# Kernel optimization log

Hardware: AMD Instinct MI355X
Metric: run time of the kernel (lower is better)

## Reference

```python
import jax, jax.numpy as jnp
import numpy as np

B, N, M, DIM, H, DH = 2, 2048, 2048, 512, 8, 64
INNER = H * DH  # 512


def setup_inputs() -> dict:
    key = jax.random.key(0)
    ks = jax.random.split(key, 9)
    s = 0.02
    return {
        "x": jax.random.normal(ks[0], (B, N, DIM), jnp.float32),
        "x1": jax.random.normal(ks[1], (B, M, DIM), jnp.float32),
        "attn_mat": jax.random.normal(ks[2], (B, H, N, M), jnp.float32),
        "dots_para": jax.random.uniform(ks[3], (1,), jnp.float32),
        "mat_para": jax.random.uniform(ks[4], (1,), jnp.float32),
        "W_qv": jax.random.normal(ks[5], (DIM, 2 * INNER), jnp.float32) * s,
        "W_k": jax.random.normal(ks[6], (DIM, INNER), jnp.float32) * s,
        "W_out": jax.random.normal(ks[7], (INNER, DIM), jnp.float32) * s,
        "b_out": jax.random.normal(ks[8], (DIM,), jnp.float32) * s,
    }


def _split_heads(t):
    # [b, n, h*d] -> [b, h, n, d]
    b, n, _ = t.shape
    return t.reshape(b, n, H, DH).transpose(0, 2, 1, 3)


def reference(x, x1, attn_mat, dots_para, mat_para, W_qv, W_k, W_out, b_out):
    scale = DH ** -0.5
    qv = x @ W_qv                      # [b, n, 2*inner]
    q, v = jnp.split(qv, 2, axis=-1)
    q = _split_heads(q)                # [b, h, n, d]
    v = _split_heads(v)                # [b, h, n, d]
    k = _split_heads(x1 @ W_k)         # [b, h, m, d]
    dots = jnp.einsum("bhnd,bhmd->bhnm", q, k) * scale
    dots = dots * dots_para + attn_mat * mat_para
    attn = jax.nn.softmax(dots, axis=-1)
    out = jnp.einsum("bhnm,bhmd->bhnd", attn, v)
    out = out.transpose(0, 2, 1, 3).reshape(x.shape[0], x.shape[1], INNER)
    return out @ W_out + b_out
```

## Files before the change

### kernel.cpp

```cpp
#include <hip/hip_runtime.h>

#define NB 2048
#define MB 2048
#define SPLITS 4
#define MSP (MB / SPLITS)

typedef __attribute__((ext_vector_type(8))) short short8;
typedef __attribute__((ext_vector_type(4))) float floatx4;

__device__ __forceinline__ unsigned short f2bf(float f) {
    union { float f; unsigned int u; } v; v.f = f;
    unsigned int r = (v.u + 0x7FFFu + ((v.u >> 16) & 1u)) >> 16;
    return (unsigned short)r;
}

__device__ __forceinline__ int swz(int row, int k) {
    return (row << 6) + ((((k >> 3) ^ (row & 7))) << 3) + (k & 7);
}
__device__ __forceinline__ int vswz(int row, int k) {
    return (row << 6) + ((((k >> 3) ^ (row & 7) ^ ((row >> 3) & 7))) << 3) + (k & 7);
}

__device__ __forceinline__ void gload16(const unsigned short* g, short* l) {
    __builtin_amdgcn_global_load_lds(
        (const __attribute__((address_space(1))) void*)g,
        (__attribute__((address_space(3))) void*)l, 16, 0, 0);
}

__launch_bounds__(256)
__global__ void prep(const float* __restrict__ x, const float* __restrict__ x1,
                     const float* __restrict__ Wqv, const float* __restrict__ Wk,
                     const float* __restrict__ Wout,
                     unsigned short* __restrict__ xb, unsigned short* __restrict__ x1b,
                     unsigned short* __restrict__ Wqvt, unsigned short* __restrict__ Wkt,
                     unsigned short* __restrict__ Woutt) {
    __shared__ float t[64][65];
    const int bid = blockIdx.x, tid = threadIdx.x;
    if (bid < 2048) {
        const float* in = bid < 1024 ? x : x1;
        unsigned short* out = bid < 1024 ? xb : x1b;
        size_t off = ((size_t)(bid & 1023) * 256 + tid) * 8;
        float4 d0 = *(const float4*)(in + off);
        float4 d1 = *(const float4*)(in + off + 4);
        uint4 o;
        o.x = (unsigned int)f2bf(d0.x) | ((unsigned int)f2bf(d0.y) << 16);
        o.y = (unsigned int)f2bf(d0.z) | ((unsigned int)f2bf(d0.w) << 16);
        o.z = (unsigned int)f2bf(d1.x) | ((unsigned int)f2bf(d1.y) << 16);
        o.w = (unsigned int)f2bf(d1.z) | ((unsigned int)f2bf(d1.w) << 16);
        *(uint4*)(out + off) = o;
        return;
    }
    int tb = bid - 2048;
    const float* W; unsigned short* Wt; int N;
    if (tb < 128)      { W = Wqv;  Wt = Wqvt;  N = 1024; }
    else if (tb < 192) { tb -= 128; W = Wk;   Wt = Wkt;   N = 512; }
    else               { tb -= 192; W = Wout; Wt = Woutt; N = 512; }
    const int k0 = (tb & 7) * 64, n0 = (tb >> 3) * 64;
#pragma unroll
    for (int p = 0; p < 4; p++) {
        int idx = p * 256 + tid;
        int kr = idx >> 4, c4 = (idx & 15) << 2;
        float4 d = *(const float4*)(W + (size_t)(k0 + kr) * N + n0 + c4);
        t[kr][c4 + 0] = d.x; t[kr][c4 + 1] = d.y; t[kr][c4 + 2] = d.z; t[kr][c4 + 3] = d.w;
    }
    __syncthreads();
#pragma unroll
    for (int p = 0; p < 4; p++) {
        int idx = p * 256 + tid;
        int nr = idx >> 4, k4 = (idx & 15) << 2;
        uint2 o;
        o.x = (unsigned int)f2bf(t[k4 + 0][nr]) | ((unsigned int)f2bf(t[k4 + 1][nr]) << 16);
        o.y = (unsigned int)f2bf(t[k4 + 2][nr]) | ((unsigned int)f2bf(t[k4 + 3][nr]) << 16);
        *(uint2*)(Wt + (size_t)(n0 + nr) * 512 + k0 + k4) = o;
    }
}

template <int OUT_BF16>
__device__ __forceinline__ void gemm128_body(const unsigned short* __restrict__ A,
                                             const unsigned short* __restrict__ Bt,
                                             const float* __restrict__ bias,
                                             void* __restrict__ Cp, int Nc, int m0, int n0,
                                             short* Al, short* Bl) {
    const int tid = threadIdx.x;
    const int w = tid >> 6, lane = tid & 63;
    const int quad = lane >> 4, c16 = lane & 15;
    const int wr = (w >> 1) * 64, wc = (w & 1) * 64;

    floatx4 acc[4][4];
#pragma unroll
    for (int i = 0; i < 4; i++)
#pragma unroll
        for (int j = 0; j < 4; j++) acc[i][j] = floatx4{0.f, 0.f, 0.f, 0.f};

    const unsigned short* Ap = A + (size_t)m0 * 512;
    const unsigned short* Bp = Bt + (size_t)n0 * 512;

    for (int kk = 0; kk < 512; kk += 64) {
#pragma unroll
        for (int p = 0; p < 4; p++) {
            int idx = p * 256 + tid;
            int row = idx >> 3, c8 = (idx & 7) << 3;
            gload16(Ap + (size_t)row * 512 + kk + c8, Al + idx * 8);
            gload16(Bp + (size_t)row * 512 + kk + c8, Bl + idx * 8);
        }
        __syncthreads();
#pragma unroll
        for (int kc = 0; kc < 2; kc++) {
            short8 af[4], bf[4];
#pragma unroll
            for (int mt = 0; mt < 4; mt++)
                af[mt] = *(const short8*)&Al[(wr + mt * 16 + c16) * 64 + kc * 32 + quad * 8];
#pragma unroll
            for (int nt = 0; nt < 4; nt++)
                bf[nt] = *(const short8*)&Bl[(wc + nt * 16 + c16) * 64 + kc * 32 + quad * 8];
#pragma unroll
            for (int mt = 0; mt < 4; mt++)
#pragma unroll
                for (int nt = 0; nt < 4; nt++)
                    acc[mt][nt] = __builtin_amdgcn_mfma_f32_16x16x32_bf16(af[mt], bf[nt], acc[mt][nt], 0, 0, 0);
        }
        __syncthreads();
    }
#pragma unroll
    for (int mt = 0; mt < 4; mt++)
#pragma unroll
        for (int nt = 0; nt < 4; nt++)
#pragma unroll
            for (int r = 0; r < 4; r++) {
                int row = m0 + wr + mt * 16 + quad * 4 + r;
                int col = n0 + wc + nt * 16 + c16;
                float v = acc[mt][nt][r];
                if (OUT_BF16) {
                    ((unsigned short*)Cp)[(size_t)row * Nc + col] = f2bf(v);
                } else {
                    ((float*)Cp)[(size_t)row * Nc + col] = v + bias[col];
                }
            }
}

__launch_bounds__(256)
__global__ void gemm_qvk(const unsigned short* __restrict__ xb, const unsigned short* __restrict__ x1b,
                         const unsigned short* __restrict__ Wqvt, const unsigned short* __restrict__ Wkt,
                         unsigned short* __restrict__ qvbf, unsigned short* __restrict__ kbf) {
    __shared__ short Al[128 * 64];
    __shared__ short Bl[128 * 64];
    int bid = blockIdx.x;
    if (bid < 256) {
        gemm128_body<1>(xb, Wqvt, nullptr, qvbf, 1024, (bid & 31) * 128, (bid >> 5) * 128, Al, Bl);
    } else {
        bid -= 256;
        gemm128_body<1>(x1b, Wkt, nullptr, kbf, 512, (bid & 31) * 128, (bid >> 5) * 128, Al, Bl);
    }
}

__launch_bounds__(256)
__global__ void gemm_out(const unsigned short* __restrict__ A, const unsigned short* __restrict__ Bt,
                         const float* __restrict__ bias, float* __restrict__ C) {
    __shared__ short Al[128 * 64];
    __shared__ short Bl[128 * 64];
    gemm128_body<0>(A, Bt, bias, C, 512, blockIdx.x * 128, blockIdx.y * 128, Al, Bl);
}

__launch_bounds__(256)
__global__ void flash_attn(const unsigned short* __restrict__ qv,
                           const unsigned short* __restrict__ kb,
                           const float* __restrict__ attn_mat,
                           const float* __restrict__ dots_para,
                           const float* __restrict__ mat_para,
                           float* __restrict__ Opart,
                           float* __restrict__ lpart) {
    __shared__ short QP[4][32 * 64];
    __shared__ short Ks[2][64 * 64];
    __shared__ short Vs[2][64 * 64];

    const int tid = threadIdx.x, w = tid >> 6, lane = tid & 63;
    const int quad = lane >> 4, c16 = lane & 15;
    const int q0 = blockIdx.x * 128;
    const int bh = blockIdx.y;
    const int sp = blockIdx.z;
    const int b = bh >> 3, h = bh & 7;
    const int ms = sp * MSP;

    const float log2e = 1.4426950408889634f;
    const float mp = mat_para[0] * log2e;
    const float sdp = dots_para[0] * 0.125f * log2e;

    short* QPf = (short*)QP;
#pragma unroll
    for (int p = 0; p < 4; p++) {
        int id = p * 256 + tid;
        int r = id >> 3, c = id & 7;
        *(uint4*)&QPf[swz(r, c * 8)] =
            *(const uint4*)(qv + (size_t)(b * NB + q0 + r) * 1024 + h * 64 + c * 8);
    }
    __syncthreads();
    short8 qf[2][2];
#pragma unroll
    for (int at = 0; at < 2; at++)
#pragma unroll
        for (int kc = 0; kc < 2; kc++)
            qf[at][kc] = *(const short8*)&QPf[swz(w * 32 + at * 16 + c16, kc * 32 + quad * 8)];
    short* Pw = &QPf[w * 2048];

    const int sr = tid >> 3, sc = tid & 7;
    uint4 kreg[2], vreg[2];
    auto loadKV = [&](int m) {
#pragma unroll
        for (int p = 0; p < 2; p++) {
            int r = p * 32 + sr;
            kreg[p] = *(const uint4*)(kb + (size_t)(b * MB + m + r) * 512 + h * 64 + sc * 8);
            vreg[p] = *(const uint4*)(qv + (size_t)(b * NB + m + r) * 1024 + 512 + h * 64 + sc * 8);
        }
    };
    auto storeKV = [&](int bufi) {
#pragma unroll
        for (int p = 0; p < 2; p++) {
            int r = p * 32 + sr;
            *(uint4*)&Ks[bufi][swz(r, sc * 8)] = kreg[p];
            uint4 d = vreg[p];
            Vs[bufi][vswz(sc * 8 + 0, r)] = (short)(d.x & 0xffff);
            Vs[bufi][vswz(sc * 8 + 1, r)] = (short)(d.x >> 16);
            Vs[bufi][vswz(sc * 8 + 2, r)] = (short)(d.y & 0xffff);
            Vs[bufi][vswz(sc * 8 + 3, r)] = (short)(d.y >> 16);
            Vs[bufi][vswz(sc * 8 + 4, r)] = (short)(d.z & 0xffff);
            Vs[bufi][vswz(sc * 8 + 5, r)] = (short)(d.z >> 16);
            Vs[bufi][vswz(sc * 8 + 6, r)] = (short)(d.w & 0xffff);
            Vs[bufi][vswz(sc * 8 + 7, r)] = (short)(d.w >> 16);
        }
    };
    const float* amp = attn_mat + ((size_t)bh * NB + q0 + w * 32 + quad * 4) * MB + c16;
    float amr[2][4][4];
    auto loadAM = [&](int m0_) {
#pragma unroll
        for (int at = 0; at < 2; at++)
#pragma unroll
            for (int r = 0; r < 4; r++)
#pragma unroll
                for (int t = 0; t < 4; t++)
                    amr[at][t][r] = amp[(size_t)(at * 16 + r) * MB + m0_ + t * 16];
    };

    loadKV(ms);
    storeKV(0);
    loadKV(ms + 64 < ms + MSP ? ms + 64 : ms);
    loadAM(ms);

    floatx4 O[2][4];
    float l[2][4];
#pragma unroll
    for (int at = 0; at < 2; at++)
#pragma unroll
        for (int i = 0; i < 4; i++) { O[at][i] = floatx4{0.f, 0.f, 0.f, 0.f}; l[at][i] = 0.f; }

    for (int it = 0; it < MSP / 64; it++) {
        const int m0 = ms + it * 64;
        const int buf = it & 1, nbuf = buf ^ 1;
        __syncthreads();
        storeKV(nbuf);
        int mnn = m0 + 128; if (mnn >= ms + MSP) mnn = ms;
        loadKV(mnn);

        floatx4 S[2][4];
        __builtin_amdgcn_s_setprio(1);
#pragma unroll
        for (int t = 0; t < 4; t++) {
            short8 kf0 = *(const short8*)&Ks[buf][swz(t * 16 + c16, quad * 8)];
            short8 kf1 = *(const short8*)&Ks[buf][swz(t * 16 + c16, 32 + quad * 8)];
#pragma unroll
            for (int at = 0; at < 2; at++) {
                floatx4 s = floatx4{0.f, 0.f, 0.f, 0.f};
                s = __builtin_amdgcn_mfma_f32_16x16x32_bf16(qf[at][0], kf0, s, 0, 0, 0);
                s = __builtin_amdgcn_mfma_f32_16x16x32_bf16(qf[at][1], kf1, s, 0, 0, 0);
                S[at][t] = s;
            }
        }
        __builtin_amdgcn_s_setprio(0);

#pragma unroll
        for (int at = 0; at < 2; at++)
#pragma unroll
            for (int t = 0; t < 4; t++) {
                float p0 = exp2f(fmaf(S[at][t][0], sdp, amr[at][t][0] * mp));
                float p1 = exp2f(fmaf(S[at][t][1], sdp, amr[at][t][1] * mp));
                float p2 = exp2f(fmaf(S[at][t][2], sdp, amr[at][t][2] * mp));
                float p3 = exp2f(fmaf(S[at][t][3], sdp, amr[at][t][3] * mp));
                l[at][0] += p0; l[at][1] += p1; l[at][2] += p2; l[at][3] += p3;
                unsigned int w01, w23;
                asm("v_cvt_pk_bf16_f32 %0, %1, %2" : "=v"(w01) : "v"(p0), "v"(p1));
                asm("v_cvt_pk_bf16_f32 %0, %1, %2" : "=v"(w23) : "v"(p2), "v"(p3));
                int br = at * 16 + quad * 4;
                Pw[swz(br + 0, t * 16 + c16)] = (short)(w01 & 0xffff);
                Pw[swz(br + 1, t * 16 + c16)] = (short)(w01 >> 16);
                Pw[swz(br + 2, t * 16 + c16)] = (short)(w23 & 0xffff);
                Pw[swz(br + 3, t * 16 + c16)] = (short)(w23 >> 16);
            }
        int mnx = m0 + 64; if (mnx >= ms + MSP) mnx = ms;
        loadAM(mnx);
        __threadfence_block();

        short8 pf[2][2];
#pragma unroll
        for (int at = 0; at < 2; at++)
#pragma unroll
            for (int kc = 0; kc < 2; kc++)
                pf[at][kc] = *(const short8*)&Pw[swz(at * 16 + c16, kc * 32 + quad * 8)];
        __builtin_amdgcn_s_setprio(1);
#pragma unroll
        for (int dt = 0; dt < 4; dt++) {
            short8 vf0 = *(const short8*)&Vs[buf][vswz(dt * 16 + c16, quad * 8)];
            short8 vf1 = *(const short8*)&Vs[buf][vswz(dt * 16 + c16, 32 + quad * 8)];
#pragma unroll
            for (int at = 0; at < 2; at++) {
                O[at][dt] = __builtin_amdgcn_mfma_f32_16x16x32_bf16(pf[at][0], vf0, O[at][dt], 0, 0, 0);
                O[at][dt] = __builtin_amdgcn_mfma_f32_16x16x32_bf16(pf[at][1], vf1, O[at][dt], 0, 0, 0);
            }
        }
        __builtin_amdgcn_s_setprio(0);
    }

#pragma unroll
    for (int at = 0; at < 2; at++) {
#pragma unroll
        for (int r = 0; r < 4; r++) {
            float s = l[at][r];
            s += __shfl_xor(s, 1);
            s += __shfl_xor(s, 2);
            s += __shfl_xor(s, 4);
            s += __shfl_xor(s, 8);
            l[at][r] = s;
        }
        if (c16 == 0) {
#pragma unroll
            for (int r = 0; r < 4; r++)
                lpart[(size_t)(sp * 16 + bh) * NB + q0 + w * 32 + at * 16 + quad * 4 + r] = l[at][r];
        }
#pragma unroll
        for (int dt = 0; dt < 4; dt++)
#pragma unroll
            for (int r = 0; r < 4; r++) {
                size_t row = (size_t)sp * 4096 + b * NB + q0 + w * 32 + at * 16 + quad * 4 + r;
                Opart[row * 512 + h * 64 + dt * 16 + c16] = O[at][dt][r];
            }
    }
}

__launch_bounds__(256)
__global__ void combine_splits(const float* __restrict__ Opart, const float* __restrict__ lpart,
                               unsigned short* __restrict__ ao) {
    int idx = blockIdx.x * 256 + threadIdx.x;
    int row = idx >> 7;
    int col = (idx & 127) << 2;
    int b = row >> 11, n = row & 2047, h = col >> 6;
    float ls = 0.f;
    float4 o = {0.f, 0.f, 0.f, 0.f};
#pragma unroll
    for (int sp = 0; sp < SPLITS; sp++) {
        ls += lpart[(size_t)(sp * 16 + b * 8 + h) * NB + n];
        float4 os = *(const float4*)(Opart + ((size_t)sp * 4096 + row) * 512 + col);
        o.x += os.x; o.y += os.y; o.z += os.z; o.w += os.w;
    }
    float rinv = 1.0f / ls;
    uint2 pk;
    pk.x = (unsigned int)f2bf(o.x * rinv) | ((unsigned int)f2bf(o.y * rinv) << 16);
    pk.y = (unsigned int)f2bf(o.z * rinv) | ((unsigned int)f2bf(o.w * rinv) << 16);
    *(uint2*)(ao + (size_t)row * 512 + col) = pk;
}

extern "C" void kernel_launch(void* const* d_in, const int* in_sizes, int n_in,
                              void* d_out, int out_size, void* d_ws, size_t ws_size,
                              hipStream_t stream) {
    const float* x         = (const float*)d_in[0];
    const float* x1        = (const float*)d_in[1];
    const float* attn_mat  = (const float*)d_in[2];
    const float* dots_para = (const float*)d_in[3];
    const float* mat_para  = (const float*)d_in[4];
    const float* W_qv      = (const float*)d_in[5];
    const float* W_k       = (const float*)d_in[6];
    const float* W_out     = (const float*)d_in[7];
    const float* b_out     = (const float*)d_in[8];
    float* out = (float*)d_out;

    unsigned short* xb    = (unsigned short*)d_ws;
    unsigned short* x1b   = xb    + (size_t)4096 * 512;
    unsigned short* qvbf  = x1b   + (size_t)4096 * 512;
    unsigned short* kbf   = qvbf  + (size_t)4096 * 1024;
    unsigned short* aobf  = kbf   + (size_t)4096 * 512;
    unsigned short* Wqvt  = aobf  + (size_t)4096 * 512;
    unsigned short* Wkt   = Wqvt  + (size_t)1024 * 512;
    unsigned short* Woutt = Wkt   + (size_t)512 * 512;
    float*          Opart = (float*)(Woutt + (size_t)512 * 512);
    float*          lpart = Opart + (size_t)SPLITS * 4096 * 512;

    dim3 blk(256);
    prep<<<2304, blk, 0, stream>>>(x, x1, W_qv, W_k, W_out, xb, x1b, Wqvt, Wkt, Woutt);
    gemm_qvk<<<384, blk, 0, stream>>>(xb, x1b, Wqvt, Wkt, qvbf, kbf);
    flash_attn<<<dim3(16, 16, SPLITS), blk, 0, stream>>>(qvbf, kbf, attn_mat, dots_para, mat_para, Opart, lpart);
    combine_splits<<<2048, blk, 0, stream>>>(Opart, lpart, aobf);
    gemm_out<<<dim3(32, 4), blk, 0, stream>>>(aobf, Woutt, b_out, out);
}
```

Baseline: 439.3 us.

## Double-buffer GEMMs with swizzled async LDS loads and halve N tile

The GEMM body now double-buffers A/B tiles in LDS using direct global-to-LDS loads with an XOR-swizzled layout, which removes one barrier per k-step and avoids bank conflicts. The N tile shrinks from 128 to 64 so twice as many blocks launch for the QVK and output GEMMs. In flash attention, Q and K tiles also use direct swizzled global-to-LDS loads instead of going through registers, while V still goes through registers for its transpose. The changes trade more LDS per block and smaller per-wave tiles for better latency hiding and more parallelism.

```diff
diff --git a/kernel.cpp b/kernel.cpp
--- a/kernel.cpp
+++ b/kernel.cpp
@@ -76,59 +76,73 @@
 }
 
 template <int OUT_BF16>
-__device__ __forceinline__ void gemm128_body(const unsigned short* __restrict__ A,
-                                             const unsigned short* __restrict__ Bt,
-                                             const float* __restrict__ bias,
-                                             void* __restrict__ Cp, int Nc, int m0, int n0,
-                                             short* Al, short* Bl) {
+__device__ __forceinline__ void gemm_body(const unsigned short* __restrict__ A,
+                                          const unsigned short* __restrict__ Bt,
+                                          const float* __restrict__ bias,
+                                          void* __restrict__ Cp, int Nc, int m0, int n0,
+                                          short* Al, short* Bl) {
     const int tid = threadIdx.x;
     const int w = tid >> 6, lane = tid & 63;
     const int quad = lane >> 4, c16 = lane & 15;
-    const int wr = (w >> 1) * 64, wc = (w & 1) * 64;
-
-    floatx4 acc[4][4];
+    const int wm = (w >> 1) * 64, wn = (w & 1) * 32;
+
+    floatx4 acc[4][2];
 #pragma unroll
     for (int i = 0; i < 4; i++)
 #pragma unroll
-        for (int j = 0; j < 4; j++) acc[i][j] = floatx4{0.f, 0.f, 0.f, 0.f};
+        for (int j = 0; j < 2; j++) acc[i][j] = floatx4{0.f, 0.f, 0.f, 0.f};
 
     const unsigned short* Ap = A + (size_t)m0 * 512;
     const unsigned short* Bp = Bt + (size_t)n0 * 512;
 
-    for (int kk = 0; kk < 512; kk += 64) {
+    auto stage = [&](int bufi, int kk) {
 #pragma unroll
         for (int p = 0; p < 4; p++) {
             int idx = p * 256 + tid;
-            int row = idx >> 3, c8 = (idx & 7) << 3;
-            gload16(Ap + (size_t)row * 512 + kk + c8, Al + idx * 8);
-            gload16(Bp + (size_t)row * 512 + kk + c8, Bl + idx * 8);
+            int row = idx >> 3, c = idx & 7;
+            gload16(Ap + (size_t)row * 512 + kk + ((c ^ (row & 7)) << 3),
+                    Al + bufi * 8192 + idx * 8);
+        }
+#pragma unroll
+        for (int p = 0; p < 2; p++) {
+            int idx = p * 256 + tid;
+            int row = idx >> 3, c = idx & 7;
+            gload16(Bp + (size_t)row * 512 + kk + ((c ^ (row & 7)) << 3),
+                    Bl + bufi * 4096 + idx * 8);
+        }
+    };
+
+    stage(0, 0);
+    __syncthreads();
+
+    for (int ks = 0; ks < 8; ks++) {
+        const int buf = ks & 1;
+        if (ks < 7) stage(buf ^ 1, (ks + 1) * 64);
+#pragma unroll
+        for (int kc = 0; kc < 2; kc++) {
+            short8 af[4], bf[2];
+#pragma unroll
+            for (int mt = 0; mt < 4; mt++)
+                af[mt] = *(const short8*)&Al[buf * 8192 + swz(wm + mt * 16 + c16, kc * 32 + quad * 8)];
+#pragma unroll
+            for (int nt = 0; nt < 2; nt++)
+                bf[nt] = *(const short8*)&Bl[buf * 4096 + swz(wn + nt * 16 + c16, kc * 32 + quad * 8)];
+#pragma unroll
+            for (int mt = 0; mt < 4; mt++)
+#pragma unroll
+                for (int nt = 0; nt < 2; nt++)
+                    acc[mt][nt] = __builtin_amdgcn_mfma_f32_16x16x32_bf16(af[mt], bf[nt], acc[mt][nt], 0, 0, 0);
         }
         __syncthreads();
-#pragma unroll
-        for (int kc = 0; kc < 2; kc++) {
-            short8 af[4], bf[4];
-#pragma unroll
-            for (int mt = 0; mt < 4; mt++)
-                af[mt] = *(const short8*)&Al[(wr + mt * 16 + c16) * 64 + kc * 32 + quad * 8];
-#pragma unroll
-            for (int nt = 0; nt < 4; nt++)
-                bf[nt] = *(const short8*)&Bl[(wc + nt * 16 + c16) * 64 + kc * 32 + quad * 8];
-#pragma unroll
-            for (int mt = 0; mt < 4; mt++)
-#pragma unroll
-                for (int nt = 0; nt < 4; nt++)
-                    acc[mt][nt] = __builtin_amdgcn_mfma_f32_16x16x32_bf16(af[mt], bf[nt], acc[mt][nt], 0, 0, 0);
-        }
-        __syncthreads();
     }
 #pragma unroll
     for (int mt = 0; mt < 4; mt++)
 #pragma unroll
-        for (int nt = 0; nt < 4; nt++)
+        for (int nt = 0; nt < 2; nt++)
 #pragma unroll
             for (int r = 0; r < 4; r++) {
-                int row = m0 + wr + mt * 16 + quad * 4 + r;
-                int col = n0 + wc + nt * 16 + c16;
+                int row = m0 + wm + mt * 16 + quad * 4 + r;
+                int col = n0 + wn + nt * 16 + c16;
                 float v = acc[mt][nt][r];
                 if (OUT_BF16) {
                     ((unsigned short*)Cp)[(size_t)row * Nc + col] = f2bf(v);
@@ -142,23 +156,23 @@
 __global__ void gemm_qvk(const unsigned short* __restrict__ xb, const unsigned short* __restrict__ x1b,
                          const unsigned short* __restrict__ Wqvt, const unsigned short* __restrict__ Wkt,
                          unsigned short* __restrict__ qvbf, unsigned short* __restrict__ kbf) {
-    __shared__ short Al[128 * 64];
-    __shared__ short Bl[128 * 64];
+    __shared__ short Al[2 * 128 * 64];
+    __shared__ short Bl[2 * 64 * 64];
     int bid = blockIdx.x;
-    if (bid < 256) {
-        gemm128_body<1>(xb, Wqvt, nullptr, qvbf, 1024, (bid & 31) * 128, (bid >> 5) * 128, Al, Bl);
+    if (bid < 512) {
+        gemm_body<1>(xb, Wqvt, nullptr, qvbf, 1024, (bid & 31) * 128, (bid >> 5) * 64, Al, Bl);
     } else {
-        bid -= 256;
-        gemm128_body<1>(x1b, Wkt, nullptr, kbf, 512, (bid & 31) * 128, (bid >> 5) * 128, Al, Bl);
+        bid -= 512;
+        gemm_body<1>(x1b, Wkt, nullptr, kbf, 512, (bid & 31) * 128, (bid >> 5) * 64, Al, Bl);
     }
 }
 
 __launch_bounds__(256)
 __global__ void gemm_out(const unsigned short* __restrict__ A, const unsigned short* __restrict__ Bt,
                          const float* __restrict__ bias, float* __restrict__ C) {
-    __shared__ short Al[128 * 64];
-    __shared__ short Bl[128 * 64];
-    gemm128_body<0>(A, Bt, bias, C, 512, blockIdx.x * 128, blockIdx.y * 128, Al, Bl);
+    __shared__ short Al[2 * 128 * 64];
+    __shared__ short Bl[2 * 64 * 64];
+    gemm_body<0>(A, Bt, bias, C, 512, blockIdx.x * 128, blockIdx.y * 64, Al, Bl);
 }
 
 __launch_bounds__(256)
@@ -186,37 +200,38 @@
     const float sdp = dots_para[0] * 0.125f * log2e;
 
     short* QPf = (short*)QP;
+    const int sr = tid >> 3, sc = tid & 7;
+
 #pragma unroll
     for (int p = 0; p < 4; p++) {
-        int id = p * 256 + tid;
-        int r = id >> 3, c = id & 7;
-        *(uint4*)&QPf[swz(r, c * 8)] =
-            *(const uint4*)(qv + (size_t)(b * NB + q0 + r) * 1024 + h * 64 + c * 8);
-    }
-    __syncthreads();
-    short8 qf[2][2];
-#pragma unroll
-    for (int at = 0; at < 2; at++)
-#pragma unroll
-        for (int kc = 0; kc < 2; kc++)
-            qf[at][kc] = *(const short8*)&QPf[swz(w * 32 + at * 16 + c16, kc * 32 + quad * 8)];
-    short* Pw = &QPf[w * 2048];
-
-    const int sr = tid >> 3, sc = tid & 7;
-    uint4 kreg[2], vreg[2];
-    auto loadKV = [&](int m) {
+        int idx = p * 256 + tid;
+        int r = idx >> 3, c = idx & 7;
+        gload16(qv + (size_t)(b * NB + q0 + r) * 1024 + h * 64 + ((c ^ (r & 7)) << 3),
+                QPf + idx * 8);
+    }
+
+    auto gloadK = [&](int bufi, int m) {
+#pragma unroll
+        for (int p = 0; p < 2; p++) {
+            int idx = p * 256 + tid;
+            int row = idx >> 3, c = idx & 7;
+            gload16(kb + (size_t)(b * MB + m + row) * 512 + h * 64 + ((c ^ (row & 7)) << 3),
+                    &Ks[bufi][idx * 8]);
+        }
+    };
+
+    uint4 vreg[2];
+    auto loadV = [&](int m) {
 #pragma unroll
         for (int p = 0; p < 2; p++) {
             int r = p * 32 + sr;
-            kreg[p] = *(const uint4*)(kb + (size_t)(b * MB + m + r) * 512 + h * 64 + sc * 8);
             vreg[p] = *(const uint4*)(qv + (size_t)(b * NB + m + r) * 1024 + 512 + h * 64 + sc * 8);
         }
     };
-    auto storeKV = [&](int bufi) {
+    auto storeV = [&](int bufi) {
 #pragma unroll
         for (int p = 0; p < 2; p++) {
             int r = p * 32 + sr;
-            *(uint4*)&Ks[bufi][swz(r, sc * 8)] = kreg[p];
             uint4 d = vreg[p];
             Vs[bufi][vswz(sc * 8 + 0, r)] = (short)(d.x & 0xffff);
             Vs[bufi][vswz(sc * 8 + 1, r)] = (short)(d.x >> 16);
@@ -240,10 +255,19 @@
                     amr[at][t][r] = amp[(size_t)(at * 16 + r) * MB + m0_ + t * 16];
     };
 
-    loadKV(ms);
-    storeKV(0);
-    loadKV(ms + 64 < ms + MSP ? ms + 64 : ms);
+    gloadK(0, ms);
+    loadV(ms);
     loadAM(ms);
+    __syncthreads();
+    short8 qf[2][2];
+#pragma unroll
+    for (int at = 0; at < 2; at++)
+#pragma unroll
+        for (int kc = 0; kc < 2; kc++)
+            qf[at][kc] = *(const short8*)&QPf[swz(w * 32 + at * 16 + c16, kc * 32 + quad * 8)];
+    short* Pw = &QPf[w * 2048];
+    storeV(0);
+    loadV(ms + 64);
 
     floatx4 O[2][4];
     float l[2][4];
@@ -256,9 +280,11 @@
         const int m0 = ms + it * 64;
         const int buf = it & 1, nbuf = buf ^ 1;
         __syncthreads();
-        storeKV(nbuf);
-        int mnn = m0 + 128; if (mnn >= ms + MSP) mnn = ms;
-        loadKV(mnn);
+        int mn1 = m0 + 64;  if (mn1 >= ms + MSP) mn1 = ms;
+        int mn2 = m0 + 128; if (mn2 >= ms + MSP) mn2 = ms;
+        gloadK(nbuf, mn1);
+        storeV(nbuf);
+        loadV(mn2);
 
         floatx4 S[2][4];
         __builtin_amdgcn_s_setprio(1);
@@ -294,8 +320,7 @@
                 Pw[swz(br + 2, t * 16 + c16)] = (short)(w23 & 0xffff);
                 Pw[swz(br + 3, t * 16 + c16)] = (short)(w23 >> 16);
             }
-        int mnx = m0 + 64; if (mnx >= ms + MSP) mnx = ms;
-        loadAM(mnx);
+        loadAM(mn1);
         __threadfence_block();
 
         short8 pf[2][2];
@@ -393,8 +418,8 @@
 
     dim3 blk(256);
     prep<<<2304, blk, 0, stream>>>(x, x1, W_qv, W_k, W_out, xb, x1b, Wqvt, Wkt, Woutt);
-    gemm_qvk<<<384, blk, 0, stream>>>(xb, x1b, Wqvt, Wkt, qvbf, kbf);
+    gemm_qvk<<<768, blk, 0, stream>>>(xb, x1b, Wqvt, Wkt, qvbf, kbf);
     flash_attn<<<dim3(16, 16, SPLITS), blk, 0, stream>>>(qvbf, kbf, attn_mat, dots_para, mat_para, Opart, lpart);
     combine_splits<<<2048, blk, 0, stream>>>(Opart, lpart, aobf);
-    gemm_out<<<dim3(32, 4), blk, 0, stream>>>(aobf, Woutt, b_out, out);
-}
+    gemm_out<<<dim3(32, 8), blk, 0, stream>>>(aobf, Woutt, b_out, out);
+}
```

Result: no change. 432.8 us (-1.5%).
